# Kernel tuning notes

Hardware: AMD Instinct MI355X
Metric: run time of the kernel (lower is better)

The kernel has to match this reference:

```python
import jax, jax.numpy as jnp
import numpy as np

DIM = 2048

def setup_inputs() -> dict:
    key = jax.random.key(0)
    k_x, k_q, k_k, k_v, k_o = jax.random.split(key, 5)
    scale = 1.0 / np.sqrt(DIM)
    x = jax.random.normal(k_x, (2, 4096, DIM), dtype=jnp.float32)
    # nn.Linear weights are [out, in]; y = x @ W^T
    wq = jax.random.normal(k_q, (DIM, DIM), dtype=jnp.float32) * scale
    wk = jax.random.normal(k_k, (DIM, DIM), dtype=jnp.float32) * scale
    wv = jax.random.normal(k_v, (DIM, DIM), dtype=jnp.float32) * scale
    wo = jax.random.normal(k_o, (DIM, DIM), dtype=jnp.float32) * scale
    return {"x": x, "wq": wq, "wk": wk, "wv": wv, "wo": wo}

def reference(x, wq, wk, wv, wo):
    # Faithful to the torch module: NO head split; full-dim QK^T, scale by sqrt(dim).
    q = jnp.einsum('bsd,ed->bse', x, wq)
    k = jnp.einsum('bsd,ed->bse', x, wk)
    v = jnp.einsum('bsd,ed->bse', x, wv)
    scores = jnp.einsum('bqd,bkd->bqk', q, k) / jnp.sqrt(jnp.asarray(DIM, x.dtype))
    attn = jax.nn.softmax(scores, axis=-1)
    ctx = jnp.einsum('bqk,bkd->bqd', attn, v)
    return jnp.einsum('bsd,ed->bse', ctx, wo)
```

## Files before the change

### kernel.cpp

```cpp
#include <hip/hip_runtime.h>
#include <hip/hip_bf16.h>
#include <stdint.h>
#include <math.h>

typedef __attribute__((ext_vector_type(4))) float f32x4;
typedef __attribute__((ext_vector_type(8))) short s16x8;

typedef const __attribute__((address_space(1))) void* gas_ptr;
typedef __attribute__((address_space(3))) void* las_ptr;

__device__ __forceinline__ float bf2f(unsigned short u) {
    union { unsigned int i; float f; } x; x.i = ((unsigned int)u) << 16; return x.f;
}
__device__ __forceinline__ unsigned short f2bf(float f) {
    union { float f; unsigned int u; } x; x.f = f;
    unsigned int r = x.u + 0x7FFFu + ((x.u >> 16) & 1u);
    return (unsigned short)(r >> 16);
}

__global__ __launch_bounds__(256) void cvt_f32_bf16(const float* __restrict__ src,
                                                    unsigned short* __restrict__ dst,
                                                    long n) {
    long i = ((long)blockIdx.x * 256 + threadIdx.x) * 8;
    if (i + 8 > n) return;
    f32x4 a = *(const f32x4*)(src + i);
    f32x4 b = *(const f32x4*)(src + i + 4);
    s16x8 o;
    o[0] = (short)f2bf(a[0]); o[1] = (short)f2bf(a[1]);
    o[2] = (short)f2bf(a[2]); o[3] = (short)f2bf(a[3]);
    o[4] = (short)f2bf(b[0]); o[5] = (short)f2bf(b[1]);
    o[6] = (short)f2bf(b[2]); o[7] = (short)f2bf(b[3]);
    *(s16x8*)(dst + i) = o;
}

template <typename CT>
__global__ __launch_bounds__(512, 2)
void gemm256_bt(const unsigned short* __restrict__ A,
                const unsigned short* __restrict__ B,
                CT* __restrict__ C,
                int N, int K, int nt,
                long sA, long sB, long sC, float alpha)
{
    A += (long)blockIdx.z * sA;
    B += (long)blockIdx.z * sB;
    C += (long)blockIdx.z * sC;

    __shared__ unsigned short L[2][2][2][128][64];

    const int t    = threadIdx.x;
    const int lane = t & 63;
    const int wid  = t >> 6;
    const int wm   = wid >> 2;
    const int wn   = wid & 3;

    const int cpx = (int)gridDim.x >> 3;
    const int bx  = ((int)blockIdx.x & 7) * cpx + ((int)blockIdx.x >> 3);
    const long brow = (long)bx * 256;
    const long bcol = (long)blockIdx.y * 256;

    const int lr = lane & 15;
    const int hi = lane >> 4;
    const int sw = (lr & 7) << 3;

    int voff[2];
    const unsigned short* pA[2][2];
    const unsigned short* pB[2][2];
    {
        const unsigned short* Ab = A + brow * K;
        const unsigned short* Bb = B + bcol * K;
        #pragma unroll
        for (int j = 0; j < 2; ++j) {
            int u  = t + 512 * j;
            int ix = u >> 3;
            int cg = u & 7;
            int cs = (cg * 8) ^ ((ix & 7) << 3);
            voff[j] = u * 8;
            long ra0 = ((long)(ix >> 6) << 7) | (0 << 6) | (ix & 63);
            long ra1 = ((long)(ix >> 6) << 7) | (1 << 6) | (ix & 63);
            long rb0 = ((long)(ix >> 5) << 6) | (0 << 5) | (ix & 31);
            long rb1 = ((long)(ix >> 5) << 6) | (1 << 5) | (ix & 31);
            pA[0][j] = Ab + ra0 * K + cs;
            pA[1][j] = Ab + ra1 * K + cs;
            pB[0][j] = Bb + rb0 * K + cs;
            pB[1][j] = Bb + rb1 * K + cs;
        }
    }

#define STAGE_A(H, KT) do { \
    _Pragma("unroll") \
    for (int j = 0; j < 2; ++j) \
        __builtin_amdgcn_global_load_lds((gas_ptr)(pA[H][j] + (long)(KT) * 64), \
            (las_ptr)(&L[(KT) & 1][0][H][0][0] + voff[j]), 16, 0, 0); \
} while (0)
#define STAGE_B(H, KT) do { \
    _Pragma("unroll") \
    for (int j = 0; j < 2; ++j) \
        __builtin_amdgcn_global_load_lds((gas_ptr)(pB[H][j] + (long)(KT) * 64), \
            (las_ptr)(&L[(KT) & 1][1][H][0][0] + voff[j]), 16, 0, 0); \
} while (0)

#define LOAD_AF(DST, CUR, QM) do { \
    _Pragma("unroll") \
    for (int m = 0; m < 4; ++m) \
        _Pragma("unroll") \
        for (int kk = 0; kk < 2; ++kk) \
            DST[m][kk] = *(const s16x8*)&L[CUR][0][QM][wm * 64 + m * 16 + lr][(kk * 32 + hi * 8) ^ sw]; \
} while (0)
#define LOAD_BQ(DST, CUR, QN) do { \
    _Pragma("unroll") \
    for (int n = 0; n < 2; ++n) \
        _Pragma("unroll") \
        for (int kk = 0; kk < 2; ++kk) \
            DST[n][kk] = *(const s16x8*)&L[CUR][1][QN][wn * 32 + n * 16 + lr][(kk * 32 + hi * 8) ^ sw]; \
} while (0)
#define MFMA_Q(QM, QN, AF, BQ) do { \
    _Pragma("unroll") \
    for (int m = 0; m < 4; ++m) \
        _Pragma("unroll") \
        for (int n = 0; n < 2; ++n) \
            _Pragma("unroll") \
            for (int kk = 0; kk < 2; ++kk) \
                acc[(QM) * 4 + m][(QN) * 2 + n] = __builtin_amdgcn_mfma_f32_16x16x32_bf16( \
                    AF[m][kk], BQ[n][kk], acc[(QM) * 4 + m][(QN) * 2 + n], 0, 0, 0); \
} while (0)

    f32x4 acc[8][4];
    #pragma unroll
    for (int m = 0; m < 8; ++m)
        #pragma unroll
        for (int n = 0; n < 4; ++n)
            acc[m][n] = {0.f, 0.f, 0.f, 0.f};

    s16x8 af0[4][2], af1[4][2], bq0[2][2], bq1[2][2];

    STAGE_A(0, 0); STAGE_B(0, 0); STAGE_A(1, 0); STAGE_B(1, 0);
    asm volatile("s_waitcnt vmcnt(0)" ::: "memory");
    __builtin_amdgcn_s_barrier();
    asm volatile("" ::: "memory");

    LOAD_AF(af0, 0, 0);
    LOAD_BQ(bq0, 0, 0);
    LOAD_BQ(bq1, 0, 1);
    if (nt > 1) {
        STAGE_A(0, 1); STAGE_B(0, 1);
        STAGE_A(1, 1); STAGE_B(1, 1);
    }
    __builtin_amdgcn_s_setprio(1);
    MFMA_Q(0, 0, af0, bq0);
    MFMA_Q(0, 1, af0, bq1);
    __builtin_amdgcn_s_setprio(0);
    LOAD_AF(af1, 0, 1);
    asm volatile("s_waitcnt lgkmcnt(0)" ::: "memory");
    asm volatile("s_waitcnt vmcnt(0)" ::: "memory");
    __builtin_amdgcn_s_barrier();
    asm volatile("" ::: "memory");

    for (int kt = 1; kt < nt; ++kt) {
        const int cur = kt & 1;
        __builtin_amdgcn_s_setprio(1);
        MFMA_Q(1, 1, af1, bq1);
        MFMA_Q(1, 0, af1, bq0);
        __builtin_amdgcn_s_setprio(0);
        LOAD_AF(af0, cur, 0);
        LOAD_BQ(bq0, cur, 0);
        LOAD_BQ(bq1, cur, 1);
        if (kt + 1 < nt) {
            STAGE_A(0, kt + 1); STAGE_B(0, kt + 1);
            STAGE_A(1, kt + 1); STAGE_B(1, kt + 1);
        }
        __builtin_amdgcn_s_setprio(1);
        MFMA_Q(0, 0, af0, bq0);
        MFMA_Q(0, 1, af0, bq1);
        __builtin_amdgcn_s_setprio(0);
        LOAD_AF(af1, cur, 1);
        asm volatile("s_waitcnt lgkmcnt(0)" ::: "memory");
        asm volatile("s_waitcnt vmcnt(0)" ::: "memory");
        __builtin_amdgcn_s_barrier();
        asm volatile("" ::: "memory");
    }
    MFMA_Q(1, 1, af1, bq1);
    MFMA_Q(1, 0, af1, bq0);
#undef STAGE_A
#undef STAGE_B
#undef LOAD_AF
#undef LOAD_BQ
#undef MFMA_Q

    #pragma unroll
    for (int m = 0; m < 8; ++m) {
        #pragma unroll
        for (int n = 0; n < 4; ++n) {
            #pragma unroll
            for (int i = 0; i < 4; ++i) {
                long row = brow + wm * 128 + m * 16 + hi * 4 + i;
                long col = bcol + wn * 64 + n * 16 + lr;
                float vv = acc[m][n][i] * alpha;
                if constexpr (sizeof(CT) == 2) {
                    ((unsigned short*)C)[row * (long)N + col] = f2bf(vv);
                } else {
                    ((float*)C)[row * (long)N + col] = vv;
                }
            }
        }
    }
}

__global__ __launch_bounds__(256) void transpose_bf16(const unsigned short* __restrict__ src,
                                                      unsigned short* __restrict__ dst,
                                                      int srows, int scols) {
    __shared__ unsigned short tile[64][66];
    const long bofs = (long)blockIdx.z * srows * scols;
    const unsigned short* s = src + bofs;
    unsigned short* d = dst + bofs;
    const int c0 = blockIdx.x * 64;
    const int r0 = blockIdx.y * 64;
    const int tx = threadIdx.x & 15;
    const int ty = threadIdx.x >> 4;

    #pragma unroll
    for (int k = 0; k < 4; ++k) {
        int r = ty + 16 * k;
        ushort4 v = *(const ushort4*)(s + (long)(r0 + r) * scols + c0 + tx * 4);
        tile[r][tx * 4 + 0] = v.x; tile[r][tx * 4 + 1] = v.y;
        tile[r][tx * 4 + 2] = v.z; tile[r][tx * 4 + 3] = v.w;
    }
    __syncthreads();
    #pragma unroll
    for (int k = 0; k < 4; ++k) {
        int dr = ty + 16 * k;
        ushort4 v;
        v.x = tile[tx * 4 + 0][dr]; v.y = tile[tx * 4 + 1][dr];
        v.z = tile[tx * 4 + 2][dr]; v.w = tile[tx * 4 + 3][dr];
        *(ushort4*)(d + (long)(c0 + dr) * srows + r0 + tx * 4) = v;
    }
}

__global__ __launch_bounds__(256) void softmax_inplace(unsigned short* __restrict__ S, int ncols) {
    const long row = blockIdx.x;
    unsigned short* p = S + row * (long)ncols;
    const int t = threadIdx.x;
    const int wid = t >> 6;

    ushort4 raw[4];
    const ushort4* pv = (const ushort4*)(p + t * 16);
    #pragma unroll
    for (int i = 0; i < 4; ++i) raw[i] = pv[i];

    float v[16];
    float mx = -1e30f;
    #pragma unroll
    for (int i = 0; i < 4; ++i) {
        v[4*i+0] = bf2f(raw[i].x); v[4*i+1] = bf2f(raw[i].y);
        v[4*i+2] = bf2f(raw[i].z); v[4*i+3] = bf2f(raw[i].w);
    }
    #pragma unroll
    for (int i = 0; i < 16; ++i) mx = fmaxf(mx, v[i]);
    #pragma unroll
    for (int off = 32; off > 0; off >>= 1) mx = fmaxf(mx, __shfl_xor(mx, off));

    __shared__ float red[8];
    if ((t & 63) == 0) red[wid] = mx;
    __syncthreads();
    mx = fmaxf(fmaxf(red[0], red[1]), fmaxf(red[2], red[3]));

    float sum = 0.f;
    #pragma unroll
    for (int i = 0; i < 16; ++i) { v[i] = __expf(v[i] - mx); sum += v[i]; }
    #pragma unroll
    for (int off = 32; off > 0; off >>= 1) sum += __shfl_xor(sum, off);
    __syncthreads();
    if ((t & 63) == 0) red[4 + wid] = sum;
    __syncthreads();
    sum = red[4] + red[5] + red[6] + red[7];
    const float inv = 1.0f / sum;

    ushort4* po = (ushort4*)(p + t * 16);
    #pragma unroll
    for (int i = 0; i < 4; ++i) {
        ushort4 o;
        o.x = f2bf(v[4*i+0] * inv); o.y = f2bf(v[4*i+1] * inv);
        o.z = f2bf(v[4*i+2] * inv); o.w = f2bf(v[4*i+3] * inv);
        po[i] = o;
    }
}

extern "C" void kernel_launch(void* const* d_in, const int* in_sizes, int n_in,
                              void* d_out, int out_size, void* d_ws, size_t ws_size,
                              hipStream_t stream) {
    const float* x  = (const float*)d_in[0];
    const float* wq = (const float*)d_in[1];
    const float* wk = (const float*)d_in[2];
    const float* wv = (const float*)d_in[3];
    const float* wo = (const float*)d_in[4];
    float* out = (float*)d_out;

    const long SDIM = 2048, SEQ = 4096, BATCH = 2;
    const long MS = BATCH * SEQ;
    const long XN = MS * SDIM;
    const long WN = SDIM * SDIM;

    unsigned short* ws  = (unsigned short*)d_ws;
    unsigned short* Xbf = ws;
    unsigned short* Wqb = ws + XN;
    unsigned short* Wkb = Wqb + WN;
    unsigned short* Wvb = Wkb + WN;
    unsigned short* Wob = Wvb + WN;
    unsigned short* Qb  = Wob + WN;
    unsigned short* Kb  = Qb + XN;
    unsigned short* Vb  = Kb + XN;
    unsigned short* Sb  = Vb + XN;
    unsigned short* Vt  = Xbf;
    unsigned short* Ctx = Qb;

    cvt_f32_bf16<<<(int)(XN / 2048), 256, 0, stream>>>(x,  Xbf, XN);
    cvt_f32_bf16<<<(int)(WN / 2048), 256, 0, stream>>>(wq, Wqb, WN);
    cvt_f32_bf16<<<(int)(WN / 2048), 256, 0, stream>>>(wk, Wkb, WN);
    cvt_f32_bf16<<<(int)(WN / 2048), 256, 0, stream>>>(wv, Wvb, WN);
    cvt_f32_bf16<<<(int)(WN / 2048), 256, 0, stream>>>(wo, Wob, WN);

    dim3 gp((unsigned)(MS / 256), (unsigned)(SDIM / 256), 1);
    gemm256_bt<unsigned short><<<gp, 512, 0, stream>>>(Xbf, Wqb, Qb, (int)SDIM, (int)SDIM, (int)(SDIM / 64), 0, 0, 0, 1.0f);
    gemm256_bt<unsigned short><<<gp, 512, 0, stream>>>(Xbf, Wkb, Kb, (int)SDIM, (int)SDIM, (int)(SDIM / 64), 0, 0, 0, 1.0f);
    gemm256_bt<unsigned short><<<gp, 512, 0, stream>>>(Xbf, Wvb, Vb, (int)SDIM, (int)SDIM, (int)(SDIM / 64), 0, 0, 0, 1.0f);

    dim3 gt((unsigned)(SDIM / 64), (unsigned)(SEQ / 64), (unsigned)BATCH);
    transpose_bf16<<<gt, 256, 0, stream>>>(Vb, Vt, (int)SEQ, (int)SDIM);

    const float scale = 1.0f / sqrtf((float)SDIM);
    dim3 gs((unsigned)(SEQ / 256), (unsigned)(SEQ / 256), (unsigned)BATCH);
    gemm256_bt<unsigned short><<<gs, 512, 0, stream>>>(Qb, Kb, Sb, (int)SEQ, (int)SDIM, (int)(SDIM / 64),
                                                       SEQ * SDIM, SEQ * SDIM, SEQ * SEQ, scale);

    softmax_inplace<<<(int)(BATCH * SEQ), 256, 0, stream>>>(Sb, (int)SEQ);

    dim3 gc((unsigned)(SEQ / 256), (unsigned)(SDIM / 256), (unsigned)BATCH);
    gemm256_bt<unsigned short><<<gc, 512, 0, stream>>>(Sb, Vt, Ctx, (int)SDIM, (int)SEQ, (int)(SEQ / 64),
                                                       SEQ * SEQ, SDIM * SEQ, SEQ * SDIM, 1.0f);

    gemm256_bt<float><<<gp, 512, 0, stream>>>(Ctx, Wob, out, (int)SDIM, (int)SDIM, (int)(SDIM / 64), 0, 0, 0, 1.0f);
}
```

Before: 538.1 us.

## Batch QKV projections into one launch and fuse V transpose into epilogue

```diff
diff --git a/kernel.cpp b/kernel.cpp
--- a/kernel.cpp
+++ b/kernel.cpp
@@ -18,34 +18,62 @@
     return (unsigned short)(r >> 16);
 }
 
-__global__ __launch_bounds__(256) void cvt_f32_bf16(const float* __restrict__ src,
-                                                    unsigned short* __restrict__ dst,
-                                                    long n) {
-    long i = ((long)blockIdx.x * 256 + threadIdx.x) * 8;
-    if (i + 8 > n) return;
+__global__ __launch_bounds__(256) void cvt5(const float* __restrict__ x,
+                                            const float* __restrict__ wq,
+                                            const float* __restrict__ wk,
+                                            const float* __restrict__ wv,
+                                            const float* __restrict__ wo,
+                                            unsigned short* __restrict__ xb,
+                                            unsigned short* __restrict__ wqb,
+                                            unsigned short* __restrict__ wkb,
+                                            unsigned short* __restrict__ wvb,
+                                            unsigned short* __restrict__ wob) {
+    int b = blockIdx.x;
+    const float* src; unsigned short* dst; long off;
+    if (b < 8192) {
+        src = x; dst = xb; off = (long)b * 2048;
+    } else {
+        int w = (b - 8192) >> 11;
+        off = (long)((b - 8192) & 2047) * 2048;
+        src = (w == 0) ? wq : (w == 1) ? wk : (w == 2) ? wv : wo;
+        dst = (w == 0) ? wqb : (w == 1) ? wkb : (w == 2) ? wvb : wob;
+    }
+    long i = off + threadIdx.x * 8;
     f32x4 a = *(const f32x4*)(src + i);
-    f32x4 b = *(const f32x4*)(src + i + 4);
+    f32x4 c = *(const f32x4*)(src + i + 4);
     s16x8 o;
     o[0] = (short)f2bf(a[0]); o[1] = (short)f2bf(a[1]);
     o[2] = (short)f2bf(a[2]); o[3] = (short)f2bf(a[3]);
-    o[4] = (short)f2bf(b[0]); o[5] = (short)f2bf(b[1]);
-    o[6] = (short)f2bf(b[2]); o[7] = (short)f2bf(b[3]);
+    o[4] = (short)f2bf(c[0]); o[5] = (short)f2bf(c[1]);
+    o[6] = (short)f2bf(c[2]); o[7] = (short)f2bf(c[3]);
     *(s16x8*)(dst + i) = o;
 }
 
-template <typename CT>
+template <typename CT, int MODE>
 __global__ __launch_bounds__(512, 2)
 void gemm256_bt(const unsigned short* __restrict__ A,
-                const unsigned short* __restrict__ B,
-                CT* __restrict__ C,
+                const unsigned short* __restrict__ B0,
+                const unsigned short* __restrict__ B1,
+                const unsigned short* __restrict__ B2,
+                CT* __restrict__ C0, CT* __restrict__ C1, CT* __restrict__ C2,
                 int N, int K, int nt,
                 long sA, long sB, long sC, float alpha)
 {
-    A += (long)blockIdx.z * sA;
-    B += (long)blockIdx.z * sB;
-    C += (long)blockIdx.z * sC;
-
-    __shared__ unsigned short L[2][2][2][128][64];
+    const unsigned short* B = B0;
+    CT* C = C0;
+    if constexpr (MODE == 1) {
+        if (blockIdx.z == 1)      { B = B1; C = C1; }
+        else if (blockIdx.z == 2) { B = B2; C = C2; }
+    } else {
+        A += (long)blockIdx.z * sA;
+        B += (long)blockIdx.z * sB;
+        C += (long)blockIdx.z * sC;
+    }
+
+    __shared__ union {
+        unsigned short L[2][2][2][128][64];
+        unsigned short T[256][264];
+    } sm;
 
     const int t    = threadIdx.x;
     const int lane = t & 63;
@@ -90,13 +118,13 @@
     _Pragma("unroll") \
     for (int j = 0; j < 2; ++j) \
         __builtin_amdgcn_global_load_lds((gas_ptr)(pA[H][j] + (long)(KT) * 64), \
-            (las_ptr)(&L[(KT) & 1][0][H][0][0] + voff[j]), 16, 0, 0); \
+            (las_ptr)(&sm.L[(KT) & 1][0][H][0][0] + voff[j]), 16, 0, 0); \
 } while (0)
 #define STAGE_B(H, KT) do { \
     _Pragma("unroll") \
     for (int j = 0; j < 2; ++j) \
         __builtin_amdgcn_global_load_lds((gas_ptr)(pB[H][j] + (long)(KT) * 64), \
-            (las_ptr)(&L[(KT) & 1][1][H][0][0] + voff[j]), 16, 0, 0); \
+            (las_ptr)(&sm.L[(KT) & 1][1][H][0][0] + voff[j]), 16, 0, 0); \
 } while (0)
 
 #define LOAD_AF(DST, CUR, QM) do { \
@@ -104,14 +132,14 @@
     for (int m = 0; m < 4; ++m) \
         _Pragma("unroll") \
         for (int kk = 0; kk < 2; ++kk) \
-            DST[m][kk] = *(const s16x8*)&L[CUR][0][QM][wm * 64 + m * 16 + lr][(kk * 32 + hi * 8) ^ sw]; \
+            DST[m][kk] = *(const s16x8*)&sm.L[CUR][0][QM][wm * 64 + m * 16 + lr][(kk * 32 + hi * 8) ^ sw]; \
 } while (0)
 #define LOAD_BQ(DST, CUR, QN) do { \
     _Pragma("unroll") \
     for (int n = 0; n < 2; ++n) \
         _Pragma("unroll") \
         for (int kk = 0; kk < 2; ++kk) \
-            DST[n][kk] = *(const s16x8*)&L[CUR][1][QN][wn * 32 + n * 16 + lr][(kk * 32 + hi * 8) ^ sw]; \
+            DST[n][kk] = *(const s16x8*)&sm.L[CUR][1][QN][wn * 32 + n * 16 + lr][(kk * 32 + hi * 8) ^ sw]; \
 } while (0)
 #define MFMA_Q(QM, QN, AF, BQ) do { \
     _Pragma("unroll") \
@@ -186,52 +214,49 @@
 #undef LOAD_BQ
 #undef MFMA_Q
 
-    #pragma unroll
-    for (int m = 0; m < 8; ++m) {
-        #pragma unroll
-        for (int n = 0; n < 4; ++n) {
+    bool transposed = false;
+    if constexpr (MODE == 1) transposed = (blockIdx.z == 2);
+
+    if (transposed) {
+        __syncthreads();
+        #pragma unroll
+        for (int m = 0; m < 8; ++m)
             #pragma unroll
-            for (int i = 0; i < 4; ++i) {
-                long row = brow + wm * 128 + m * 16 + hi * 4 + i;
-                long col = bcol + wn * 64 + n * 16 + lr;
-                float vv = acc[m][n][i] * alpha;
-                if constexpr (sizeof(CT) == 2) {
-                    ((unsigned short*)C)[row * (long)N + col] = f2bf(vv);
-                } else {
-                    ((float*)C)[row * (long)N + col] = vv;
+            for (int n = 0; n < 4; ++n)
+                #pragma unroll
+                for (int i = 0; i < 4; ++i)
+                    sm.T[wn * 64 + n * 16 + lr][wm * 128 + m * 16 + hi * 4 + i] =
+                        f2bf(acc[m][n][i]);
+        __syncthreads();
+        const int  bz = (int)(brow >> 12);
+        const long s0 = brow & 4095;
+        unsigned short* vt = (unsigned short*)C + (long)bz * 2048 * 4096;
+        #pragma unroll
+        for (int k = 0; k < 16; ++k) {
+            int c = t + 512 * k;
+            int d = c >> 5;
+            int s = (c & 31) * 8;
+            s16x8 v = *(const s16x8*)&sm.T[d][s];
+            *(s16x8*)(vt + (bcol + d) * 4096L + s0 + s) = v;
+        }
+    } else {
+        #pragma unroll
+        for (int m = 0; m < 8; ++m) {
+            #pragma unroll
+            for (int n = 0; n < 4; ++n) {
+                #pragma unroll
+                for (int i = 0; i < 4; ++i) {
+                    long row = brow + wm * 128 + m * 16 + hi * 4 + i;
+                    long col = bcol + wn * 64 + n * 16 + lr;
+                    float vv = acc[m][n][i] * alpha;
+                    if constexpr (sizeof(CT) == 2) {
+                        ((unsigned short*)C)[row * (long)N + col] = f2bf(vv);
+                    } else {
+                        ((float*)C)[row * (long)N + col] = vv;
+                    }
                 }
             }
         }
-    }
-}
-
-__global__ __launch_bounds__(256) void transpose_bf16(const unsigned short* __restrict__ src,
-                                                      unsigned short* __restrict__ dst,
-                                                      int srows, int scols) {
-    __shared__ unsigned short tile[64][66];
-    const long bofs = (long)blockIdx.z * srows * scols;
-    const unsigned short* s = src + bofs;
-    unsigned short* d = dst + bofs;
-    const int c0 = blockIdx.x * 64;
-    const int r0 = blockIdx.y * 64;
-    const int tx = threadIdx.x & 15;
-    const int ty = threadIdx.x >> 4;
-
-    #pragma unroll
-    for (int k = 0; k < 4; ++k) {
-        int r = ty + 16 * k;
-        ushort4 v = *(const ushort4*)(s + (long)(r0 + r) * scols + c0 + tx * 4);
-        tile[r][tx * 4 + 0] = v.x; tile[r][tx * 4 + 1] = v.y;
-        tile[r][tx * 4 + 2] = v.z; tile[r][tx * 4 + 3] = v.w;
-    }
-    __syncthreads();
-    #pragma unroll
-    for (int k = 0; k < 4; ++k) {
-        int dr = ty + 16 * k;
-        ushort4 v;
-        v.x = tile[tx * 4 + 0][dr]; v.y = tile[tx * 4 + 1][dr];
-        v.z = tile[tx * 4 + 2][dr]; v.w = tile[tx * 4 + 3][dr];
-        *(ushort4*)(d + (long)(c0 + dr) * srows + r0 + tx * 4) = v;
     }
 }
 
@@ -307,35 +332,34 @@
     unsigned short* Wob = Wvb + WN;
     unsigned short* Qb  = Wob + WN;
     unsigned short* Kb  = Qb + XN;
-    unsigned short* Vb  = Kb + XN;
-    unsigned short* Sb  = Vb + XN;
-    unsigned short* Vt  = Xbf;
+    unsigned short* Vt  = Kb + XN;
+    unsigned short* Sb  = Vt + XN;
     unsigned short* Ctx = Qb;
 
-    cvt_f32_bf16<<<(int)(XN / 2048), 256, 0, stream>>>(x,  Xbf, XN);
-    cvt_f32_bf16<<<(int)(WN / 2048), 256, 0, stream>>>(wq, Wqb, WN);
-    cvt_f32_bf16<<<(int)(WN / 2048), 256, 0, stream>>>(wk, Wkb, WN);
-    cvt_f32_bf16<<<(int)(WN / 2048), 256, 0, stream>>>(wv, Wvb, WN);
-    cvt_f32_bf16<<<(int)(WN / 2048), 256, 0, stream>>>(wo, Wob, WN);
-
-    dim3 gp((unsigned)(MS / 256), (unsigned)(SDIM / 256), 1);
-    gemm256_bt<unsigned short><<<gp, 512, 0, stream>>>(Xbf, Wqb, Qb, (int)SDIM, (int)SDIM, (int)(SDIM / 64), 0, 0, 0, 1.0f);
-    gemm256_bt<unsigned short><<<gp, 512, 0, stream>>>(Xbf, Wkb, Kb, (int)SDIM, (int)SDIM, (int)(SDIM / 64), 0, 0, 0, 1.0f);
-    gemm256_bt<unsigned short><<<gp, 512, 0, stream>>>(Xbf, Wvb, Vb, (int)SDIM, (int)SDIM, (int)(SDIM / 64), 0, 0, 0, 1.0f);
-
-    dim3 gt((unsigned)(SDIM / 64), (unsigned)(SEQ / 64), (unsigned)BATCH);
-    transpose_bf16<<<gt, 256, 0, stream>>>(Vb, Vt, (int)SEQ, (int)SDIM);
+    cvt5<<<16384, 256, 0, stream>>>(x, wq, wk, wv, wo, Xbf, Wqb, Wkb, Wvb, Wob);
+
+    dim3 gqkv((unsigned)(MS / 256), (unsigned)(SDIM / 256), 3);
+    gemm256_bt<unsigned short, 1><<<gqkv, 512, 0, stream>>>(
+        Xbf, Wqb, Wkb, Wvb, Qb, Kb, Vt,
+        (int)SDIM, (int)SDIM, (int)(SDIM / 64), 0, 0, 0, 1.0f);
 
     const float scale = 1.0f / sqrtf((float)SDIM);
     dim3 gs((unsigned)(SEQ / 256), (unsigned)(SEQ / 256), (unsigned)BATCH);
-    gemm256_bt<unsigned short><<<gs, 512, 0, stream>>>(Qb, Kb, Sb, (int)SEQ, (int)SDIM, (int)(SDIM / 64),
-                                                       SEQ * SDIM, SEQ * SDIM, SEQ * SEQ, scale);
+    gemm256_bt<unsigned short, 0><<<gs, 512, 0, stream>>>(
+        Qb, Kb, nullptr, nullptr, Sb, nullptr, nullptr,
+        (int)SEQ, (int)SDIM, (int)(SDIM / 64),
+        SEQ * SDIM, SEQ * SDIM, SEQ * SEQ, scale);
 
     softmax_inplace<<<(int)(BATCH * SEQ), 256, 0, stream>>>(Sb, (int)SEQ);
 
     dim3 gc((unsigned)(SEQ / 256), (unsigned)(SDIM / 256), (unsigned)BATCH);
-    gemm256_bt<unsigned short><<<gc, 512, 0, stream>>>(Sb, Vt, Ctx, (int)SDIM, (int)SEQ, (int)(SEQ / 64),
-                                                       SEQ * SEQ, SDIM * SEQ, SEQ * SDIM, 1.0f);
-
-    gemm256_bt<float><<<gp, 512, 0, stream>>>(Ctx, Wob, out, (int)SDIM, (int)SDIM, (int)(SDIM / 64), 0, 0, 0, 1.0f);
-}
+    gemm256_bt<unsigned short, 0><<<gc, 512, 0, stream>>>(
+        Sb, Vt, nullptr, nullptr, Ctx, nullptr, nullptr,
+        (int)SDIM, (int)SEQ, (int)(SEQ / 64),
+        SEQ * SEQ, SDIM * SEQ, SEQ * SDIM, 1.0f);
+
+    dim3 gp((unsigned)(MS / 256), (unsigned)(SDIM / 256), 1);
+    gemm256_bt<float, 0><<<gp, 512, 0, stream>>>(
+        Ctx, Wob, nullptr, nullptr, out, nullptr, nullptr,
+        (int)SDIM, (int)SDIM, (int)(SDIM / 64), 0, 0, 0, 1.0f);
+}
```

Result: faster. 512.6 us (-4.8%).
